# Optimization experiments

Measured on AMD Instinct MI355X. Metric: run time of the kernel, lower is better.

The kernel has to match this reference:

```python
import jax, jax.numpy as jnp
import numpy as np

EPS = 1e-08
STEPS_START = 0
STEPS_END = 500


def setup_inputs() -> dict:
    key = jax.random.key(0)
    k_x, k_w, k_beta, k_b = jax.random.split(key, 4)
    B, T, D_in, D_out = 64, 500, 1024, 128
    x = jax.random.normal(k_x, (B, T, D_in), dtype=jnp.float32)
    # w ~ N(w_init_mean, w_init_std * sqrt(1/input_shape))
    w = jax.random.normal(k_w, (D_in, D_out), dtype=jnp.float32) * np.sqrt(1.0 / D_in)
    beta = jax.random.uniform(k_beta, (D_out,), dtype=jnp.float32)  # clamped to [0,1] in torch
    b = jax.random.uniform(k_b, (D_out,), dtype=jnp.float32)        # clamped >= 0 in torch
    return {"x": x, "w": w, "beta": beta, "b": b}


def reference(x, w, beta, b):
    # x: [B, T, D_in], w: [D_in, D_out], beta/b: [D_out]
    h = jnp.einsum('btc,cd->btd', x, w)          # [B, T, D_out]
    norm = jnp.sum(w * w, axis=0)                # [D_out]

    one_minus_beta = 1.0 - beta

    def step(mem, h_t):
        mem = mem * beta + one_minus_beta * h_t  # Leaky_Neuron=True
        return mem, mem

    mem0 = jnp.zeros((x.shape[0], w.shape[1]), dtype=x.dtype)
    _, mem_rec = jax.lax.scan(step, mem0, jnp.swapaxes(h, 0, 1))  # [T, B, D_out]
    mem_rec = jnp.swapaxes(mem_rec, 0, 1)                          # [B, T, D_out]

    # time_reduction == 'mean'
    output = jnp.mean(mem_rec[:, STEPS_START:STEPS_END, :], axis=1) / (norm + EPS) - b
    return output
```

## Files before the change

### kernel.cpp

```cpp
#include <hip/hip_runtime.h>
#include <hip/hip_bf16.h>

#define B_    64
#define T_    500
#define DIN   1024
#define DOUT  128
#define EPSV  1e-8f
#define BM    128
#define BK    64
#define NKC   2
#define KCL   (DIN / NKC)
#define NKT   (KCL / BK)
#define TILES 4
#define NGEMM (B_ * TILES * NKC)
#define NPREP 32

typedef __attribute__((ext_vector_type(8))) short bf16x8;
typedef __attribute__((ext_vector_type(4))) float f32x4;

#define OFF_NORM  262144
#define OFF_PART  278528

__device__ inline short f2bf(float f) {
    __hip_bfloat16 h = __float2bfloat16(f);
    return __builtin_bit_cast(short, h);
}

__device__ inline void block_sync_lds() {
    asm volatile("s_waitcnt lgkmcnt(0)" ::: "memory");
    __builtin_amdgcn_s_barrier();
    asm volatile("" ::: "memory");
}

__global__ __launch_bounds__(512) void prep_kernel(
    const float* __restrict__ w, __hip_bfloat16* __restrict__ wT,
    float* __restrict__ normPart)
{
    const int tid = threadIdx.x;
    const int blk = blockIdx.x;
    const int t   = blk * 512 + tid;
    const int d   = t & 127;
    const int kq  = t >> 7;
    float v[8];
    float ss = 0.f;
#pragma unroll
    for (int m = 0; m < 8; ++m) {
        v[m] = w[(size_t)(kq * 8 + m) * DOUT + d];
        ss += v[m] * v[m];
    }
    bf16x8 o;
#pragma unroll
    for (int m = 0; m < 8; ++m) o[m] = f2bf(v[m]);
    *reinterpret_cast<bf16x8*>(wT + (size_t)d * DIN + kq * 8) = o;

    __shared__ float red[512];
    red[tid] = ss;
    __syncthreads();
    if (tid < 128)
        normPart[blk * DOUT + tid] = red[tid] + red[tid + 128] + red[tid + 256] + red[tid + 384];
}

__global__ __launch_bounds__(512, 4) void gemm_kernel(
    const float* __restrict__ x, const float* __restrict__ beta,
    const __hip_bfloat16* __restrict__ wT, float* __restrict__ partials)
{
    __shared__ __align__(16) char smem[2 * 32768];

    const int tid  = threadIdx.x;
    const int wid  = tid >> 6;
    const int lane = tid & 63;
    const int wg   = blockIdx.x;
    const int kc   = wg & 1;
    const int tile = (wg >> 1) & 3;
    const int b    = wg >> 3;
    const int t0   = tile * BM;
    const int kbase = kc * KCL;
    const int arow = lane & 15;
    const int kblk = lane >> 4;
    const int wr   = wid >> 2;
    const int wc   = wid & 3;

    const float* xb = x + (size_t)b * T_ * DIN + kbase;

    const int sr = tid >> 4;
    const int sc = tid & 15;
    const float* ag[4];
    int awoff[4];
#pragma unroll
    for (int p = 0; p < 4; ++p) {
        int row  = p * 32 + sr;
        int trow = t0 + row; if (trow >= T_) trow = T_ - 1;
        ag[p] = xb + (size_t)trow * DIN + sc * 4;
        awoff[p] = (row * 128 + sc * 8) ^ ((row & 7) << 4);
    }
    const int bcol = tid >> 2;
    const int bch0 = (tid & 3) * 2;
    const __hip_bfloat16* bg0 = wT + (size_t)bcol * DIN + kbase + bch0 * 8;
    const __hip_bfloat16* bg1 = bg0 + 8;
    const int bwoff0 = (bcol * 128 + bch0 * 16)        ^ ((bcol & 7) << 4);
    const int bwoff1 = (bcol * 128 + (bch0 + 1) * 16)  ^ ((bcol & 7) << 4);

    int aro[4][2], bro[2][2];
#pragma unroll
    for (int fm = 0; fm < 4; ++fm)
#pragma unroll
        for (int kk = 0; kk < 2; ++kk) {
            int row = wr * 64 + fm * 16 + arow;
            aro[fm][kk] = (row * 128 + kk * 64 + kblk * 16) ^ ((row & 7) << 4);
        }
#pragma unroll
    for (int fn = 0; fn < 2; ++fn)
#pragma unroll
        for (int kk = 0; kk < 2; ++kk) {
            int col = wc * 32 + fn * 16 + arow;
            bro[fn][kk] = (col * 128 + kk * 64 + kblk * 16) ^ ((col & 7) << 4);
        }

    f32x4 acc[4][2] = {};

#define DECL_SET(S) float4 S##a0, S##a1, S##a2, S##a3; bf16x8 S##b0, S##b1;
#define LOAD_SET(S, KB) \
    S##a0 = *reinterpret_cast<const float4*>(ag[0] + (KB)); \
    S##a1 = *reinterpret_cast<const float4*>(ag[1] + (KB)); \
    S##a2 = *reinterpret_cast<const float4*>(ag[2] + (KB)); \
    S##a3 = *reinterpret_cast<const float4*>(ag[3] + (KB)); \
    S##b0 = *reinterpret_cast<const bf16x8*>(bg0 + (KB));   \
    S##b1 = *reinterpret_cast<const bf16x8*>(bg1 + (KB));
#define WRITE_SET(S, AB, BB) { \
    short4 h0; h0.x=f2bf(S##a0.x); h0.y=f2bf(S##a0.y); h0.z=f2bf(S##a0.z); h0.w=f2bf(S##a0.w); \
    *reinterpret_cast<short4*>((AB) + awoff[0]) = h0; \
    short4 h1; h1.x=f2bf(S##a1.x); h1.y=f2bf(S##a1.y); h1.z=f2bf(S##a1.z); h1.w=f2bf(S##a1.w); \
    *reinterpret_cast<short4*>((AB) + awoff[1]) = h1; \
    short4 h2; h2.x=f2bf(S##a2.x); h2.y=f2bf(S##a2.y); h2.z=f2bf(S##a2.z); h2.w=f2bf(S##a2.w); \
    *reinterpret_cast<short4*>((AB) + awoff[2]) = h2; \
    short4 h3; h3.x=f2bf(S##a3.x); h3.y=f2bf(S##a3.y); h3.z=f2bf(S##a3.z); h3.w=f2bf(S##a3.w); \
    *reinterpret_cast<short4*>((AB) + awoff[3]) = h3; \
    *reinterpret_cast<bf16x8*>((BB) + bwoff0) = S##b0; \
    *reinterpret_cast<bf16x8*>((BB) + bwoff1) = S##b1; }
#define COMPUTE(AB, BB) { \
    _Pragma("unroll") \
    for (int kk = 0; kk < 2; ++kk) { \
        bf16x8 bf0 = *reinterpret_cast<const bf16x8*>((BB) + bro[0][kk]); \
        bf16x8 bf1 = *reinterpret_cast<const bf16x8*>((BB) + bro[1][kk]); \
        _Pragma("unroll") \
        for (int fm = 0; fm < 4; ++fm) { \
            bf16x8 af = *reinterpret_cast<const bf16x8*>((AB) + aro[fm][kk]); \
            acc[fm][0] = __builtin_amdgcn_mfma_f32_16x16x32_bf16(af, bf0, acc[fm][0], 0, 0, 0); \
            acc[fm][1] = __builtin_amdgcn_mfma_f32_16x16x32_bf16(af, bf1, acc[fm][1], 0, 0, 0); \
        } } }

    DECL_SET(qe_)
    DECL_SET(qo_)

    LOAD_SET(qe_, 0)
    LOAD_SET(qo_, BK)
    WRITE_SET(qe_, smem, smem + 16384)
    block_sync_lds();

#pragma unroll
    for (int kt = 0; kt < NKT; ++kt) {
        char* Acur = smem + (kt & 1) * 32768;
        char* Bcur = Acur + 16384;
        char* Anxt = smem + ((kt + 1) & 1) * 32768;
        char* Bnxt = Anxt + 16384;

        if (kt + 2 < NKT) {
            if (kt & 1) { LOAD_SET(qo_, (kt + 2) * BK) }
            else        { LOAD_SET(qe_, (kt + 2) * BK) }
        }

        COMPUTE(Acur, Bcur)

        if (kt + 1 < NKT) {
            if (kt & 1) { WRITE_SET(qe_, Anxt, Bnxt) }
            else        { WRITE_SET(qo_, Anxt, Bnxt) }
            block_sync_lds();
        }
    }
#undef DECL_SET
#undef LOAD_SET
#undef WRITE_SET
#undef COMPUTE

    const int col0 = wc * 32 + arow;
    const int col1 = col0 + 16;
    const float lb0 = log2f(beta[col0]);
    const float lb1 = log2f(beta[col1]);
    float s0 = 0.f, s1 = 0.f;
#pragma unroll
    for (int fm = 0; fm < 4; ++fm) {
#pragma unroll
        for (int r = 0; r < 4; ++r) {
            int t = t0 + wr * 64 + fm * 16 + kblk * 4 + r;
            if (t < T_) {
                float e = (float)(T_ - t);
                s0 += (1.f - exp2f(e * lb0)) * acc[fm][0][r];
                s1 += (1.f - exp2f(e * lb1)) * acc[fm][1][r];
            }
        }
    }
    s0 += __shfl_xor(s0, 16); s0 += __shfl_xor(s0, 32);
    s1 += __shfl_xor(s1, 16); s1 += __shfl_xor(s1, 32);

    if (kblk == 0) {
        float* p = partials + ((((size_t)b * TILES + tile) * 2 + wr) * NKC + kc) * DOUT;
        p[col0] = s0;
        p[col1] = s1;
    }
}

__global__ __launch_bounds__(256) void finalize_kernel(
    const float* __restrict__ partials, const float* __restrict__ normPart,
    const float* __restrict__ bias, float* __restrict__ out)
{
    int i = blockIdx.x * 256 + threadIdx.x;
    int b = i >> 7, d = i & 127;
    float nrm = 0.f;
#pragma unroll
    for (int g = 0; g < NPREP; ++g)
        nrm += normPart[g * DOUT + d];
    float scale = 1.f / ((nrm + EPSV) * (float)T_);
    float s = 0.f;
#pragma unroll
    for (int p = 0; p < TILES * 2 * NKC; ++p)
        s += partials[((size_t)b * TILES * 2 * NKC + p) * DOUT + d];
    out[i] = s * scale - bias[d];
}

extern "C" void kernel_launch(void* const* d_in, const int* in_sizes, int n_in,
                              void* d_out, int out_size, void* d_ws, size_t ws_size,
                              hipStream_t stream) {
    const float* x    = (const float*)d_in[0];
    const float* w    = (const float*)d_in[1];
    const float* beta = (const float*)d_in[2];
    const float* bias = (const float*)d_in[3];
    float* out = (float*)d_out;

    char* ws = (char*)d_ws;
    __hip_bfloat16* wT = (__hip_bfloat16*)(ws);
    float* normPart = (float*)(ws + OFF_NORM);
    float* partials = (float*)(ws + OFF_PART);

    prep_kernel<<<NPREP, 512, 0, stream>>>(w, wT, normPart);
    gemm_kernel<<<NGEMM, 512, 0, stream>>>(x, beta, wT, partials);
    finalize_kernel<<<(B_ * DOUT) / 256, 256, 0, stream>>>(partials, normPart, bias, out);
}
```

Measured before the change: 34.17 us.

## Preload whole W slice into LDS and stream A directly from global into MFMA

The GEMM kernel now copies its full bf16 weight slice (128 columns x 256 k) into padded LDS once, then each wave loads its own 16 rows of x straight from global memory into registers, converts them to bf16 and feeds MFMAs with no A staging and no per-iteration barriers. The K split goes from 2 to 4, doubling the workgroup count, and per-block partials are reduced across waves in LDS so that one row per block is written instead of two. This removes LDS round-trips for A and the double-buffer synchronisation, in exchange for uncoalesced-ish per-lane global loads of x and a larger upfront LDS fill of B.

```diff
diff --git a/kernel.cpp b/kernel.cpp
--- a/kernel.cpp
+++ b/kernel.cpp
@@ -7,13 +7,13 @@
 #define DOUT  128
 #define EPSV  1e-8f
 #define BM    128
-#define BK    64
-#define NKC   2
+#define NKC   4
 #define KCL   (DIN / NKC)
-#define NKT   (KCL / BK)
+#define NST   (KCL / 32)
 #define TILES 4
 #define NGEMM (B_ * TILES * NKC)
 #define NPREP 32
+#define BCOLB 528
 
 typedef __attribute__((ext_vector_type(8))) short bf16x8;
 typedef __attribute__((ext_vector_type(4))) float f32x4;
@@ -24,12 +24,6 @@
 __device__ inline short f2bf(float f) {
     __hip_bfloat16 h = __float2bfloat16(f);
     return __builtin_bit_cast(short, h);
-}
-
-__device__ inline void block_sync_lds() {
-    asm volatile("s_waitcnt lgkmcnt(0)" ::: "memory");
-    __builtin_amdgcn_s_barrier();
-    asm volatile("" ::: "memory");
 }
 
 __global__ __launch_bounds__(512) void prep_kernel(
@@ -64,148 +58,88 @@
     const float* __restrict__ x, const float* __restrict__ beta,
     const __hip_bfloat16* __restrict__ wT, float* __restrict__ partials)
 {
-    __shared__ __align__(16) char smem[2 * 32768];
+    __shared__ __align__(16) char bsh[DOUT * BCOLB];
+    __shared__ float red[8][DOUT];
 
     const int tid  = threadIdx.x;
     const int wid  = tid >> 6;
     const int lane = tid & 63;
+    const int arow = lane & 15;
+    const int kblk = lane >> 4;
+
     const int wg   = blockIdx.x;
-    const int kc   = wg & 1;
-    const int tile = (wg >> 1) & 3;
-    const int b    = wg >> 3;
+    const int kc   = wg & 3;
+    const int tile = (wg >> 2) & 3;
+    const int b    = wg >> 4;
     const int t0   = tile * BM;
     const int kbase = kc * KCL;
-    const int arow = lane & 15;
-    const int kblk = lane >> 4;
-    const int wr   = wid >> 2;
-    const int wc   = wid & 3;
 
-    const float* xb = x + (size_t)b * T_ * DIN + kbase;
+    {
+        const int col = tid >> 2;
+        const int c4  = tid & 3;
+        const __hip_bfloat16* src = wT + (size_t)col * DIN + kbase;
+#pragma unroll
+        for (int j = 0; j < 8; ++j) {
+            int e = c4 * 8 + j * 32;
+            bf16x8 v = *reinterpret_cast<const bf16x8*>(src + e);
+            *reinterpret_cast<bf16x8*>(bsh + col * BCOLB + e * 2) = v;
+        }
+    }
+    __syncthreads();
 
-    const int sr = tid >> 4;
-    const int sc = tid & 15;
-    const float* ag[4];
-    int awoff[4];
+    const int trow_raw = t0 + wid * 16 + arow;
+    const int trow = trow_raw < T_ ? trow_raw : T_ - 1;
+    const float* ax = x + ((size_t)b * T_ + trow) * DIN + kbase + kblk * 8;
+
+    int bro[8];
 #pragma unroll
-    for (int p = 0; p < 4; ++p) {
-        int row  = p * 32 + sr;
-        int trow = t0 + row; if (trow >= T_) trow = T_ - 1;
-        ag[p] = xb + (size_t)trow * DIN + sc * 4;
-        awoff[p] = (row * 128 + sc * 8) ^ ((row & 7) << 4);
+    for (int fn = 0; fn < 8; ++fn)
+        bro[fn] = (fn * 16 + arow) * BCOLB + kblk * 16;
+
+    f32x4 acc[8] = {};
+
+    float4 a0 = *reinterpret_cast<const float4*>(ax);
+    float4 a1 = *reinterpret_cast<const float4*>(ax + 4);
+#pragma unroll
+    for (int s = 0; s < NST; ++s) {
+        float4 n0, n1;
+        if (s + 1 < NST) {
+            n0 = *reinterpret_cast<const float4*>(ax + (s + 1) * 32);
+            n1 = *reinterpret_cast<const float4*>(ax + (s + 1) * 32 + 4);
+        }
+        bf16x8 af;
+        af[0] = f2bf(a0.x); af[1] = f2bf(a0.y); af[2] = f2bf(a0.z); af[3] = f2bf(a0.w);
+        af[4] = f2bf(a1.x); af[5] = f2bf(a1.y); af[6] = f2bf(a1.z); af[7] = f2bf(a1.w);
+#pragma unroll
+        for (int fn = 0; fn < 8; ++fn) {
+            bf16x8 bf = *reinterpret_cast<const bf16x8*>(bsh + bro[fn] + s * 64);
+            acc[fn] = __builtin_amdgcn_mfma_f32_16x16x32_bf16(af, bf, acc[fn], 0, 0, 0);
+        }
+        if (s + 1 < NST) { a0 = n0; a1 = n1; }
     }
-    const int bcol = tid >> 2;
-    const int bch0 = (tid & 3) * 2;
-    const __hip_bfloat16* bg0 = wT + (size_t)bcol * DIN + kbase + bch0 * 8;
-    const __hip_bfloat16* bg1 = bg0 + 8;
-    const int bwoff0 = (bcol * 128 + bch0 * 16)        ^ ((bcol & 7) << 4);
-    const int bwoff1 = (bcol * 128 + (bch0 + 1) * 16)  ^ ((bcol & 7) << 4);
-
-    int aro[4][2], bro[2][2];
-#pragma unroll
-    for (int fm = 0; fm < 4; ++fm)
-#pragma unroll
-        for (int kk = 0; kk < 2; ++kk) {
-            int row = wr * 64 + fm * 16 + arow;
-            aro[fm][kk] = (row * 128 + kk * 64 + kblk * 16) ^ ((row & 7) << 4);
-        }
-#pragma unroll
-    for (int fn = 0; fn < 2; ++fn)
-#pragma unroll
-        for (int kk = 0; kk < 2; ++kk) {
-            int col = wc * 32 + fn * 16 + arow;
-            bro[fn][kk] = (col * 128 + kk * 64 + kblk * 16) ^ ((col & 7) << 4);
-        }
-
-    f32x4 acc[4][2] = {};
-
-#define DECL_SET(S) float4 S##a0, S##a1, S##a2, S##a3; bf16x8 S##b0, S##b1;
-#define LOAD_SET(S, KB) \
-    S##a0 = *reinterpret_cast<const float4*>(ag[0] + (KB)); \
-    S##a1 = *reinterpret_cast<const float4*>(ag[1] + (KB)); \
-    S##a2 = *reinterpret_cast<const float4*>(ag[2] + (KB)); \
-    S##a3 = *reinterpret_cast<const float4*>(ag[3] + (KB)); \
-    S##b0 = *reinterpret_cast<const bf16x8*>(bg0 + (KB));   \
-    S##b1 = *reinterpret_cast<const bf16x8*>(bg1 + (KB));
-#define WRITE_SET(S, AB, BB) { \
-    short4 h0; h0.x=f2bf(S##a0.x); h0.y=f2bf(S##a0.y); h0.z=f2bf(S##a0.z); h0.w=f2bf(S##a0.w); \
-    *reinterpret_cast<short4*>((AB) + awoff[0]) = h0; \
-    short4 h1; h1.x=f2bf(S##a1.x); h1.y=f2bf(S##a1.y); h1.z=f2bf(S##a1.z); h1.w=f2bf(S##a1.w); \
-    *reinterpret_cast<short4*>((AB) + awoff[1]) = h1; \
-    short4 h2; h2.x=f2bf(S##a2.x); h2.y=f2bf(S##a2.y); h2.z=f2bf(S##a2.z); h2.w=f2bf(S##a2.w); \
-    *reinterpret_cast<short4*>((AB) + awoff[2]) = h2; \
-    short4 h3; h3.x=f2bf(S##a3.x); h3.y=f2bf(S##a3.y); h3.z=f2bf(S##a3.z); h3.w=f2bf(S##a3.w); \
-    *reinterpret_cast<short4*>((AB) + awoff[3]) = h3; \
-    *reinterpret_cast<bf16x8*>((BB) + bwoff0) = S##b0; \
-    *reinterpret_cast<bf16x8*>((BB) + bwoff1) = S##b1; }
-#define COMPUTE(AB, BB) { \
-    _Pragma("unroll") \
-    for (int kk = 0; kk < 2; ++kk) { \
-        bf16x8 bf0 = *reinterpret_cast<const bf16x8*>((BB) + bro[0][kk]); \
-        bf16x8 bf1 = *reinterpret_cast<const bf16x8*>((BB) + bro[1][kk]); \
-        _Pragma("unroll") \
-        for (int fm = 0; fm < 4; ++fm) { \
-            bf16x8 af = *reinterpret_cast<const bf16x8*>((AB) + aro[fm][kk]); \
-            acc[fm][0] = __builtin_amdgcn_mfma_f32_16x16x32_bf16(af, bf0, acc[fm][0], 0, 0, 0); \
-            acc[fm][1] = __builtin_amdgcn_mfma_f32_16x16x32_bf16(af, bf1, acc[fm][1], 0, 0, 0); \
-        } } }
-
-    DECL_SET(qe_)
-    DECL_SET(qo_)
-
-    LOAD_SET(qe_, 0)
-    LOAD_SET(qo_, BK)
-    WRITE_SET(qe_, smem, smem + 16384)
-    block_sync_lds();
 
 #pragma unroll
-    for (int kt = 0; kt < NKT; ++kt) {
-        char* Acur = smem + (kt & 1) * 32768;
-        char* Bcur = Acur + 16384;
-        char* Anxt = smem + ((kt + 1) & 1) * 32768;
-        char* Bnxt = Anxt + 16384;
-
-        if (kt + 2 < NKT) {
-            if (kt & 1) { LOAD_SET(qo_, (kt + 2) * BK) }
-            else        { LOAD_SET(qe_, (kt + 2) * BK) }
-        }
-
-        COMPUTE(Acur, Bcur)
-
-        if (kt + 1 < NKT) {
-            if (kt & 1) { WRITE_SET(qe_, Anxt, Bnxt) }
-            else        { WRITE_SET(qo_, Anxt, Bnxt) }
-            block_sync_lds();
-        }
-    }
-#undef DECL_SET
-#undef LOAD_SET
-#undef WRITE_SET
-#undef COMPUTE
-
-    const int col0 = wc * 32 + arow;
-    const int col1 = col0 + 16;
-    const float lb0 = log2f(beta[col0]);
-    const float lb1 = log2f(beta[col1]);
-    float s0 = 0.f, s1 = 0.f;
-#pragma unroll
-    for (int fm = 0; fm < 4; ++fm) {
+    for (int fn = 0; fn < 8; ++fn) {
+        const int col = fn * 16 + arow;
+        const float lb = log2f(beta[col]);
+        float s = 0.f;
 #pragma unroll
         for (int r = 0; r < 4; ++r) {
-            int t = t0 + wr * 64 + fm * 16 + kblk * 4 + r;
-            if (t < T_) {
-                float e = (float)(T_ - t);
-                s0 += (1.f - exp2f(e * lb0)) * acc[fm][0][r];
-                s1 += (1.f - exp2f(e * lb1)) * acc[fm][1][r];
-            }
+            int t = t0 + wid * 16 + kblk * 4 + r;
+            if (t < T_)
+                s += (1.f - exp2f((float)(T_ - t) * lb)) * acc[fn][r];
         }
+        s += __shfl_xor(s, 16);
+        s += __shfl_xor(s, 32);
+        if (kblk == 0) red[wid][col] = s;
     }
-    s0 += __shfl_xor(s0, 16); s0 += __shfl_xor(s0, 32);
-    s1 += __shfl_xor(s1, 16); s1 += __shfl_xor(s1, 32);
+    __syncthreads();
 
-    if (kblk == 0) {
-        float* p = partials + ((((size_t)b * TILES + tile) * 2 + wr) * NKC + kc) * DOUT;
-        p[col0] = s0;
-        p[col1] = s1;
+    if (tid < DOUT) {
+        float v = 0.f;
+#pragma unroll
+        for (int ww = 0; ww < 8; ++ww) v += red[ww][tid];
+        partials[(((size_t)b * TILES + tile) * NKC + kc) * DOUT + tid] = v;
     }
 }
 
@@ -222,8 +156,8 @@
     float scale = 1.f / ((nrm + EPSV) * (float)T_);
     float s = 0.f;
 #pragma unroll
-    for (int p = 0; p < TILES * 2 * NKC; ++p)
-        s += partials[((size_t)b * TILES * 2 * NKC + p) * DOUT + d];
+    for (int p = 0; p < TILES * NKC; ++p)
+        s += partials[((size_t)b * TILES * NKC + p) * DOUT + d];
     out[i] = s * scale - bias[d];
 }
 
```

After: 41.94 us (median of 2 runs). 22.7% more time.

## Stage B weight tiles directly into LDS via global_load_lds with pre-swizzled layout

Applied to the files above, without the earlier changes.

The prep kernel now writes the bf16 transposed weights in a tile-blocked, pre-swizzled layout. The GEMM then loads B tiles straight from global memory into LDS with global_load_lds, so they no longer pass through registers and ds_write. This frees VGPRs and cuts LDS write instructions, but it needs manual vmcnt waits to order the async B loads with the register-staged A loads, and that ordering is fragile.

```diff
diff --git a/kernel.cpp b/kernel.cpp
--- a/kernel.cpp
+++ b/kernel.cpp
@@ -32,6 +32,12 @@
     asm volatile("" ::: "memory");
 }
 
+__device__ inline void gload_lds16(const void* g, void* l) {
+    __builtin_amdgcn_global_load_lds(
+        (const __attribute__((address_space(1))) void*)g,
+        (__attribute__((address_space(3))) void*)l, 16, 0, 0);
+}
+
 __global__ __launch_bounds__(512) void prep_kernel(
     const float* __restrict__ w, __hip_bfloat16* __restrict__ wT,
     float* __restrict__ normPart)
@@ -51,7 +57,7 @@
     bf16x8 o;
 #pragma unroll
     for (int m = 0; m < 8; ++m) o[m] = f2bf(v[m]);
-    *reinterpret_cast<bf16x8*>(wT + (size_t)d * DIN + kq * 8) = o;
+    *reinterpret_cast<bf16x8*>(wT + (size_t)(kq >> 3) * 8192 + d * 64 + (kq & 7) * 8) = o;
 
     __shared__ float red[512];
     red[tid] = ss;
@@ -74,13 +80,12 @@
     const int tile = (wg >> 1) & 3;
     const int b    = wg >> 3;
     const int t0   = tile * BM;
-    const int kbase = kc * KCL;
     const int arow = lane & 15;
     const int kblk = lane >> 4;
     const int wr   = wid >> 2;
     const int wc   = wid & 3;
 
-    const float* xb = x + (size_t)b * T_ * DIN + kbase;
+    const float* xb = x + (size_t)b * T_ * DIN + kc * KCL;
 
     const int sr = tid >> 4;
     const int sc = tid & 15;
@@ -93,12 +98,9 @@
         ag[p] = xb + (size_t)trow * DIN + sc * 4;
         awoff[p] = (row * 128 + sc * 8) ^ ((row & 7) << 4);
     }
-    const int bcol = tid >> 2;
-    const int bch0 = (tid & 3) * 2;
-    const __hip_bfloat16* bg0 = wT + (size_t)bcol * DIN + kbase + bch0 * 8;
-    const __hip_bfloat16* bg1 = bg0 + 8;
-    const int bwoff0 = (bcol * 128 + bch0 * 16)        ^ ((bcol & 7) << 4);
-    const int bwoff1 = (bcol * 128 + (bch0 + 1) * 16)  ^ ((bcol & 7) << 4);
+
+    const int boff0 = (wid * 16 + (lane >> 3)) * 64 + (((lane & 7) ^ (lane >> 3)) * 8);
+    const __hip_bfloat16* wTb = wT + (size_t)(kc * NKT) * 8192 + boff0;
 
     int aro[4][2], bro[2][2];
 #pragma unroll
@@ -118,15 +120,18 @@
 
     f32x4 acc[4][2] = {};
 
-#define DECL_SET(S) float4 S##a0, S##a1, S##a2, S##a3; bf16x8 S##b0, S##b1;
-#define LOAD_SET(S, KB) \
+#define STAGE_B(KT, BB) { \
+    const __hip_bfloat16* s0 = wTb + (size_t)(KT) * 8192; \
+    gload_lds16(s0,       (BB) + wid * 2048); \
+    gload_lds16(s0 + 512, (BB) + wid * 2048 + 1024); }
+
+#define DECL_SET(S) float4 S##a0, S##a1, S##a2, S##a3;
+#define LOAD_A(S, KB) \
     S##a0 = *reinterpret_cast<const float4*>(ag[0] + (KB)); \
     S##a1 = *reinterpret_cast<const float4*>(ag[1] + (KB)); \
     S##a2 = *reinterpret_cast<const float4*>(ag[2] + (KB)); \
-    S##a3 = *reinterpret_cast<const float4*>(ag[3] + (KB)); \
-    S##b0 = *reinterpret_cast<const bf16x8*>(bg0 + (KB));   \
-    S##b1 = *reinterpret_cast<const bf16x8*>(bg1 + (KB));
-#define WRITE_SET(S, AB, BB) { \
+    S##a3 = *reinterpret_cast<const float4*>(ag[3] + (KB));
+#define WRITE_A(S, AB) { \
     short4 h0; h0.x=f2bf(S##a0.x); h0.y=f2bf(S##a0.y); h0.z=f2bf(S##a0.z); h0.w=f2bf(S##a0.w); \
     *reinterpret_cast<short4*>((AB) + awoff[0]) = h0; \
     short4 h1; h1.x=f2bf(S##a1.x); h1.y=f2bf(S##a1.y); h1.z=f2bf(S##a1.z); h1.w=f2bf(S##a1.w); \
@@ -134,9 +139,7 @@
     short4 h2; h2.x=f2bf(S##a2.x); h2.y=f2bf(S##a2.y); h2.z=f2bf(S##a2.z); h2.w=f2bf(S##a2.w); \
     *reinterpret_cast<short4*>((AB) + awoff[2]) = h2; \
     short4 h3; h3.x=f2bf(S##a3.x); h3.y=f2bf(S##a3.y); h3.z=f2bf(S##a3.z); h3.w=f2bf(S##a3.w); \
-    *reinterpret_cast<short4*>((AB) + awoff[3]) = h3; \
-    *reinterpret_cast<bf16x8*>((BB) + bwoff0) = S##b0; \
-    *reinterpret_cast<bf16x8*>((BB) + bwoff1) = S##b1; }
+    *reinterpret_cast<short4*>((AB) + awoff[3]) = h3; }
 #define COMPUTE(AB, BB) { \
     _Pragma("unroll") \
     for (int kk = 0; kk < 2; ++kk) { \
@@ -148,13 +151,16 @@
             acc[fm][0] = __builtin_amdgcn_mfma_f32_16x16x32_bf16(af, bf0, acc[fm][0], 0, 0, 0); \
             acc[fm][1] = __builtin_amdgcn_mfma_f32_16x16x32_bf16(af, bf1, acc[fm][1], 0, 0, 0); \
         } } }
-
-    DECL_SET(qe_)
-    DECL_SET(qo_)
-
-    LOAD_SET(qe_, 0)
-    LOAD_SET(qo_, BK)
-    WRITE_SET(qe_, smem, smem + 16384)
+#define VMCNT(N) asm volatile("s_waitcnt vmcnt(" #N ")" ::: "memory");
+
+    DECL_SET(qe_) DECL_SET(qo_)
+
+    STAGE_B(0, smem + 16384)
+    STAGE_B(1, smem + 32768 + 16384)
+    LOAD_A(qe_, 0)
+    LOAD_A(qo_, BK)
+    WRITE_A(qe_, smem)
+    VMCNT(8)
     block_sync_lds();
 
 #pragma unroll
@@ -164,23 +170,27 @@
         char* Anxt = smem + ((kt + 1) & 1) * 32768;
         char* Bnxt = Anxt + 16384;
 
+        if (kt >= 1 && kt + 1 < NKT) { STAGE_B(kt + 1, Bnxt) }
         if (kt + 2 < NKT) {
-            if (kt & 1) { LOAD_SET(qo_, (kt + 2) * BK) }
-            else        { LOAD_SET(qe_, (kt + 2) * BK) }
+            if (kt & 1) { LOAD_A(qo_, (kt + 2) * BK) }
+            else        { LOAD_A(qe_, (kt + 2) * BK) }
         }
 
         COMPUTE(Acur, Bcur)
 
         if (kt + 1 < NKT) {
-            if (kt & 1) { WRITE_SET(qe_, Anxt, Bnxt) }
-            else        { WRITE_SET(qo_, Anxt, Bnxt) }
+            if (kt & 1) { WRITE_A(qe_, Anxt) }
+            else        { WRITE_A(qo_, Anxt) }
+            if (kt + 2 < NKT) { VMCNT(8) } else { VMCNT(0) }
             block_sync_lds();
         }
     }
+#undef STAGE_B
 #undef DECL_SET
-#undef LOAD_SET
-#undef WRITE_SET
+#undef LOAD_A
+#undef WRITE_A
 #undef COMPUTE
+#undef VMCNT
 
     const int col0 = wc * 32 + arow;
     const int col1 = col0 + 16;
```

Result: no change. 34.07 us (-0.3%).
